# Kernel optimization log

Measured on AMD Instinct MI355X. Metric: run time of the kernel, lower is better.

The kernel has to match this reference:

```python
import jax, jax.numpy as jnp
import numpy as np

N_NODES = 140000   # 14 frames * 10000 nodes/frame
N_EDGES = 2240000  # avg degree 16
NFEAT = 128
NHID = 128
N_FRAMES = 14


def setup_inputs() -> dict:
    key = jax.random.key(0)
    k1, k2, k3, k4, k5 = jax.random.split(key, 5)
    x = jax.random.normal(k1, (N_NODES, NFEAT), dtype=jnp.float32)
    # gc1 parameters (only layer actually used in forward)
    W = jax.random.normal(k2, (NFEAT, NHID), dtype=jnp.float32) * 0.05
    b = jnp.zeros((NHID,), dtype=jnp.float32)
    # sparse normalized adjacency as COO edge list (row sorted for fast segment_sum)
    edge_row = jnp.sort(jax.random.randint(k3, (N_EDGES,), 0, N_NODES, dtype=jnp.int32))
    edge_col = jax.random.randint(k4, (N_EDGES,), 0, N_NODES, dtype=jnp.int32)
    edge_val = jax.random.uniform(k5, (N_EDGES,), dtype=jnp.float32)
    return {"x": x, "W": W, "b": b, "edge_val": edge_val,
            "edge_row": edge_row, "edge_col": edge_col}


def reference(x, W, b, edge_val, edge_row, edge_col):
    # GraphConvolution: adj @ (x @ W) + b  (adj sparse, COO)
    support = x @ W                                   # [N, NHID]
    msgs = edge_val[:, None] * support[edge_col]      # [E, NHID] gather
    agg = jax.ops.segment_sum(msgs, edge_row, num_segments=N_NODES,
                              indices_are_sorted=True)  # [N, NHID] scatter-add
    h = jax.nn.relu(agg + b)
    # view(14, -1, c) then max over frame axis
    h = h.reshape(N_FRAMES, -1, NHID)                 # [14, N/14, NHID]
    h = jnp.max(h, axis=0)                            # [N/14, NHID]
    return jax.nn.log_softmax(h, axis=1)
```

## Files before the change

kernel.cpp:

```cpp
#include <hip/hip_runtime.h>
#include <hip/hip_bf16.h>

#define N_NODES 140000
#define N_EDGES 2240000
#define NFEAT 128
#define NHID 128
#define N_FRAMES 14
#define NODES_PER_FRAME 10000
#define CAP 352

typedef __attribute__((ext_vector_type(8))) short frag_b16;
typedef __attribute__((ext_vector_type(4))) int frag_i4;
typedef __attribute__((ext_vector_type(4))) float f32x4;

__device__ __forceinline__ unsigned short f2bf(float f) {
    union { float f; unsigned int u; } v; v.f = f;
    unsigned int r = v.u + 0x7fffu + ((v.u >> 16) & 1u);
    return (unsigned short)(r >> 16);
}
__device__ __forceinline__ int pk_bf16(float a, float b) {
    union { __hip_bfloat162 h; int i; } u;
    u.h = __float22bfloat162_rn(make_float2(a, b));
    return u.i;
}
__device__ __forceinline__ float2 bf2x2(unsigned int u) {
    union { unsigned int u; float f; } lo, hi;
    lo.u = u << 16;
    hi.u = u & 0xffff0000u;
    return make_float2(lo.f, hi.f);
}

__global__ void prep_kernel(const float* __restrict__ W, unsigned short* __restrict__ WT,
                            const int* __restrict__ edge_row, int* __restrict__ row_ptr) {
    int e = blockIdx.x * blockDim.x + threadIdx.x;
    if (e < NFEAT * NHID) {
        int k = e >> 7, n = e & 127;
        WT[n * 128 + k] = f2bf(W[e]);
    }
    if (e < N_EDGES) {
        int r = edge_row[e];
        int prev = (e == 0) ? -1 : edge_row[e - 1];
        for (int q = prev + 1; q <= r; ++q) row_ptr[q] = e;
        if (e == N_EDGES - 1) {
            for (int q = r + 1; q <= N_NODES; ++q) row_ptr[q] = N_EDGES;
        }
    }
}

#define WT_STRIDE 136

__global__ __launch_bounds__(256) void gemm_kernel(
        const float* __restrict__ x, const unsigned short* __restrict__ WT,
        unsigned short* __restrict__ support) {
    __shared__ unsigned short wt_lds[128 * WT_STRIDE];

    const uint4* WTv = (const uint4*)WT;
    for (int idx = threadIdx.x; idx < 2048; idx += 256) {
        uint4 d = WTv[idx];
        int elem = idx << 3;
        int n = elem >> 7, k = elem & 127;
        *(uint4*)&wt_lds[n * WT_STRIDE + k] = d;
    }

    int wave = threadIdx.x >> 6;
    int lane = threadIdx.x & 63;
    int m = lane & 15;
    int q = lane >> 4;

    long row0 = (long)blockIdx.x * 64 + wave * 16;

    int arow = (int)row0 + m;
    if (arow >= N_NODES) arow = N_NODES - 1;
    const float* xrow = x + (long)arow * 128 + q * 8;
    frag_b16 xa[4];
#pragma unroll
    for (int ks = 0; ks < 4; ++ks) {
        float4 lo = *(const float4*)(xrow + ks * 32);
        float4 hi = *(const float4*)(xrow + ks * 32 + 4);
        union { frag_b16 f; frag_i4 i; } u;
        u.i[0] = pk_bf16(lo.x, lo.y);
        u.i[1] = pk_bf16(lo.z, lo.w);
        u.i[2] = pk_bf16(hi.x, hi.y);
        u.i[3] = pk_bf16(hi.z, hi.w);
        xa[ks] = u.f;
    }

    __syncthreads();

    if (row0 < N_NODES) {
        f32x4 acc[8];
#pragma unroll
        for (int t = 0; t < 8; ++t) acc[t] = (f32x4){0.f, 0.f, 0.f, 0.f};

#pragma unroll
        for (int t = 0; t < 8; ++t) {
            const unsigned short* bp = &wt_lds[(t * 16 + m) * WT_STRIDE + q * 8];
#pragma unroll
            for (int ks = 0; ks < 4; ++ks) {
                frag_b16 wfrag = *(const frag_b16*)(bp + ks * 32);
                acc[t] = __builtin_amdgcn_mfma_f32_16x16x32_bf16(wfrag, xa[ks], acc[t], 0, 0, 0);
            }
        }

        long node = row0 + m;
        if (node < N_NODES) {
            unsigned short* srow = support + node * 128;
#pragma unroll
            for (int t = 0; t < 8; ++t) {
                int2 pk;
                pk.x = pk_bf16(acc[t][0], acc[t][1]);
                pk.y = pk_bf16(acc[t][2], acc[t][3]);
                *(int2*)(srow + t * 16 + q * 4) = pk;
            }
        }
    }
}

__global__ __launch_bounds__(128) void agg_kernel(
        const unsigned short* __restrict__ support, const float* __restrict__ b,
        const float* __restrict__ edge_val, const int* __restrict__ edge_col,
        const int* __restrict__ row_ptr, float* __restrict__ out) {
    __shared__ int   segStart[2][8];
    __shared__ int   segLen[2][8];
    __shared__ int   segOff[2][8];
    __shared__ int2  eBuf[2][CAP];
    __shared__ float xch[2][64][2];

    const int i = blockIdx.x;
    const int lane = threadIdx.x & 63;
    const int w = threadIdx.x >> 6;
    const char* supB = (const char*)support;
    const unsigned lane4 = (unsigned)lane * 4u;

    int a = 0, len = 0;
    if (lane < 7) {
        int n = (w * 7 + lane) * NODES_PER_FRAME + i;
        a = row_ptr[n];
        len = row_ptr[n + 1] - a;
    }
    int len8 = (len + 7) & ~7;
    int off = 0;
#pragma unroll
    for (int f2 = 0; f2 < 7; ++f2) {
        int L2 = __shfl(len8, f2);
        if (f2 < lane) off += L2;
    }
    if (lane < 7) { segStart[w][lane] = a; segLen[w][lane] = len; segOff[w][lane] = off; }
    if (lane == 6) segOff[w][7] = off + len8;
    __syncthreads();

    const bool fit = segOff[w][7] <= CAP;

    if (fit) {
#pragma unroll 1
        for (int f = 0; f < 7; ++f) {
            int g = segStart[w][f], s = segOff[w][f], L = segLen[w][f];
            int L8 = (L + 7) & ~7;
            for (int j = lane; j < L8; j += 64) {
                int2 v;
                if (j < L) { v.x = edge_col[g + j]; v.y = __float_as_int(edge_val[g + j]); }
                else       { v.x = 0; v.y = 0; }
                eBuf[w][s + j] = v;
            }
        }
    }
    __syncthreads();

    const float2 bb = *(const float2*)&b[lane * 2];
    float2 mx = make_float2(0.f, 0.f);

    if (fit) {
#pragma unroll 1
        for (int f = 0; f < 7; ++f) {
            int s = segOff[w][f];
            int e8 = s + ((segLen[w][f] + 7) & ~7);
            float ax = 0.f, ay = 0.f;
            for (int j = s; j < e8; j += 8) {
                unsigned sv[8];
                float vv[8];
#pragma unroll
                for (int u = 0; u < 8; ++u) {
                    int2 ed = eBuf[w][j + u];
                    unsigned o = ((unsigned)ed.x << 8) + lane4;
                    sv[u] = *(const unsigned*)(supB + o);
                    vv[u] = __int_as_float(ed.y);
                }
#pragma unroll
                for (int u = 0; u < 8; ++u) {
                    float2 s2 = bf2x2(sv[u]);
                    ax = fmaf(vv[u], s2.x, ax);
                    ay = fmaf(vv[u], s2.y, ay);
                }
            }
            float hx = ax + bb.x, hy = ay + bb.y;
            mx.x = fmaxf(mx.x, hx > 0.f ? hx : 0.f);
            mx.y = fmaxf(mx.y, hy > 0.f ? hy : 0.f);
        }
    } else {
#pragma unroll 1
        for (int f = 0; f < 7; ++f) {
            int g = segStart[w][f], L = segLen[w][f];
            float ax = 0.f, ay = 0.f;
            for (int j = 0; j < L; ++j) {
                int c = edge_col[g + j];
                float v = edge_val[g + j];
                float2 s2 = bf2x2(*(const unsigned*)(supB + (((unsigned)c << 8) + lane4)));
                ax = fmaf(v, s2.x, ax);
                ay = fmaf(v, s2.y, ay);
            }
            float hx = ax + bb.x, hy = ay + bb.y;
            mx.x = fmaxf(mx.x, hx > 0.f ? hx : 0.f);
            mx.y = fmaxf(mx.y, hy > 0.f ? hy : 0.f);
        }
    }

    xch[w][lane][0] = mx.x;
    xch[w][lane][1] = mx.y;
    __syncthreads();
    float ox = fmaxf(xch[0][lane][0], xch[1][lane][0]);
    float oy = fmaxf(xch[0][lane][1], xch[1][lane][1]);

    float M = fmaxf(ox, oy);
#pragma unroll
    for (int o = 32; o >= 1; o >>= 1) M = fmaxf(M, __shfl_xor(M, o));
    float S = __expf(ox - M) + __expf(oy - M);
#pragma unroll
    for (int o = 32; o >= 1; o >>= 1) S += __shfl_xor(S, o);

    if (w == 0) {
        float ls = __logf(S);
        float2 o2 = make_float2((ox - M) - ls, (oy - M) - ls);
        *(float2*)&out[i * 128 + lane * 2] = o2;
    }
}

extern "C" void kernel_launch(void* const* d_in, const int* in_sizes, int n_in,
                              void* d_out, int out_size, void* d_ws, size_t ws_size,
                              hipStream_t stream) {
    const float* x        = (const float*)d_in[0];
    const float* W        = (const float*)d_in[1];
    const float* b        = (const float*)d_in[2];
    const float* edge_val = (const float*)d_in[3];
    const int*   edge_row = (const int*)d_in[4];
    const int*   edge_col = (const int*)d_in[5];
    float* out = (float*)d_out;

    char* ws = (char*)d_ws;
    unsigned short* support = (unsigned short*)ws;
    unsigned short* WT      = (unsigned short*)(ws + 35840000);
    int*            row_ptr = (int*)(ws + 35840000 + 32768);

    prep_kernel<<<(N_EDGES + 255) / 256, 256, 0, stream>>>(W, WT, edge_row, row_ptr);
    gemm_kernel<<<(N_NODES + 63) / 64, 256, 0, stream>>>(x, WT, support);
    agg_kernel<<<NODES_PER_FRAME, 128, 0, stream>>>(support, b, edge_val, edge_col, row_ptr, out);
}
```

Measured before the change: 221.4 us.

## Interleave seven frame segments per wave with software-pipelined gathers in aggregation

The aggregation kernel now stages each frame's edges into a fixed-size per-frame LDS slot array of 48 entries, replacing the variable-offset packed buffer and its prefix-sum and barrier. Each wave then walks all seven frame segments in lockstep, two edges per segment per step, and prefetches the next step's support rows before doing the current FMAs. This gives 14 independent gathers in flight per iteration and hides memory latency better than the serial per-frame loop. In exchange, short segments do padded zero work up to the longest segment, register pressure rises, and any wave with a segment longer than 48 takes the slow fallback path.

Result: slower. 226.6 us (+2.4%).

```diff
diff --git a/kernel.cpp b/kernel.cpp
--- a/kernel.cpp
+++ b/kernel.cpp
@@ -7,7 +7,7 @@
 #define NHID 128
 #define N_FRAMES 14
 #define NODES_PER_FRAME 10000
-#define CAP 352
+#define FSLOTS 48
 
 typedef __attribute__((ext_vector_type(8))) short frag_b16;
 typedef __attribute__((ext_vector_type(4))) int frag_i4;
@@ -120,17 +120,13 @@
         const unsigned short* __restrict__ support, const float* __restrict__ b,
         const float* __restrict__ edge_val, const int* __restrict__ edge_col,
         const int* __restrict__ row_ptr, float* __restrict__ out) {
-    __shared__ int   segStart[2][8];
-    __shared__ int   segLen[2][8];
-    __shared__ int   segOff[2][8];
-    __shared__ int2  eBuf[2][CAP];
+    __shared__ int2  eBuf[2][7][FSLOTS];
     __shared__ float xch[2][64][2];
 
     const int i = blockIdx.x;
     const int lane = threadIdx.x & 63;
     const int w = threadIdx.x >> 6;
-    const char* supB = (const char*)support;
-    const unsigned lane4 = (unsigned)lane * 4u;
+    const unsigned int* sup32 = (const unsigned int*)support;
 
     int a = 0, len = 0;
     if (lane < 7) {
@@ -138,80 +134,99 @@
         a = row_ptr[n];
         len = row_ptr[n + 1] - a;
     }
-    int len8 = (len + 7) & ~7;
-    int off = 0;
-#pragma unroll
-    for (int f2 = 0; f2 < 7; ++f2) {
-        int L2 = __shfl(len8, f2);
-        if (f2 < lane) off += L2;
-    }
-    if (lane < 7) { segStart[w][lane] = a; segLen[w][lane] = len; segOff[w][lane] = off; }
-    if (lane == 6) segOff[w][7] = off + len8;
-    __syncthreads();
-
-    const bool fit = segOff[w][7] <= CAP;
+    int ml = len;
+    ml = max(ml, __shfl_xor(ml, 1));
+    ml = max(ml, __shfl_xor(ml, 2));
+    ml = max(ml, __shfl_xor(ml, 4));
+    const int maxlen = __shfl(ml, 0);
+    const bool fit = maxlen <= FSLOTS;
 
     if (fit) {
+#pragma unroll
+        for (int f = 0; f < 7; ++f) {
+            int aF = __shfl(a, f), lF = __shfl(len, f);
+            if (lane < FSLOTS) {
+                int2 v = make_int2(0, 0);
+                if (lane < lF) {
+                    v.x = edge_col[aF + lane];
+                    v.y = __float_as_int(edge_val[aF + lane]);
+                }
+                eBuf[w][f][lane] = v;
+            }
+        }
+    }
+
+    const float2 bb = *(const float2*)&b[lane * 2];
+    float accx[7], accy[7];
+#pragma unroll
+    for (int f = 0; f < 7; ++f) { accx[f] = 0.f; accy[f] = 0.f; }
+
+    if (fit) {
+        const int R = (maxlen + 1) >> 1;
+        int4 cur[7];
+        unsigned sv0[7], sv1[7];
+
+#pragma unroll
+        for (int f = 0; f < 7; ++f) cur[f] = *(const int4*)&eBuf[w][f][0];
+#pragma unroll
+        for (int f = 0; f < 7; ++f) {
+            sv0[f] = sup32[((unsigned)cur[f].x << 6) | lane];
+            sv1[f] = sup32[((unsigned)cur[f].z << 6) | lane];
+        }
+
 #pragma unroll 1
-        for (int f = 0; f < 7; ++f) {
-            int g = segStart[w][f], s = segOff[w][f], L = segLen[w][f];
-            int L8 = (L + 7) & ~7;
-            for (int j = lane; j < L8; j += 64) {
-                int2 v;
-                if (j < L) { v.x = edge_col[g + j]; v.y = __float_as_int(edge_val[g + j]); }
-                else       { v.x = 0; v.y = 0; }
-                eBuf[w][s + j] = v;
-            }
-        }
-    }
-    __syncthreads();
-
-    const float2 bb = *(const float2*)&b[lane * 2];
-    float2 mx = make_float2(0.f, 0.f);
-
-    if (fit) {
-#pragma unroll 1
-        for (int f = 0; f < 7; ++f) {
-            int s = segOff[w][f];
-            int e8 = s + ((segLen[w][f] + 7) & ~7);
-            float ax = 0.f, ay = 0.f;
-            for (int j = s; j < e8; j += 8) {
-                unsigned sv[8];
-                float vv[8];
-#pragma unroll
-                for (int u = 0; u < 8; ++u) {
-                    int2 ed = eBuf[w][j + u];
-                    unsigned o = ((unsigned)ed.x << 8) + lane4;
-                    sv[u] = *(const unsigned*)(supB + o);
-                    vv[u] = __int_as_float(ed.y);
-                }
-#pragma unroll
-                for (int u = 0; u < 8; ++u) {
-                    float2 s2 = bf2x2(sv[u]);
-                    ax = fmaf(vv[u], s2.x, ax);
-                    ay = fmaf(vv[u], s2.y, ay);
-                }
-            }
-            float hx = ax + bb.x, hy = ay + bb.y;
-            mx.x = fmaxf(mx.x, hx > 0.f ? hx : 0.f);
-            mx.y = fmaxf(mx.y, hy > 0.f ? hy : 0.f);
+        for (int r = 0; r < R; ++r) {
+            int ro = (r + 1) * 2;
+            if (ro > FSLOTS - 2) ro = FSLOTS - 2;
+            int4 nxt[7];
+            unsigned nv0[7], nv1[7];
+#pragma unroll
+            for (int f = 0; f < 7; ++f) nxt[f] = *(const int4*)&eBuf[w][f][ro];
+#pragma unroll
+            for (int f = 0; f < 7; ++f) {
+                nv0[f] = sup32[((unsigned)nxt[f].x << 6) | lane];
+                nv1[f] = sup32[((unsigned)nxt[f].z << 6) | lane];
+            }
+#pragma unroll
+            for (int f = 0; f < 7; ++f) {
+                float v0 = __int_as_float(cur[f].y);
+                float v1 = __int_as_float(cur[f].w);
+                float2 s0 = bf2x2(sv0[f]);
+                float2 s1 = bf2x2(sv1[f]);
+                accx[f] = fmaf(v0, s0.x, accx[f]);
+                accy[f] = fmaf(v0, s0.y, accy[f]);
+                accx[f] = fmaf(v1, s1.x, accx[f]);
+                accy[f] = fmaf(v1, s1.y, accy[f]);
+            }
+#pragma unroll
+            for (int f = 0; f < 7; ++f) {
+                cur[f] = nxt[f];
+                sv0[f] = nv0[f];
+                sv1[f] = nv1[f];
+            }
         }
     } else {
 #pragma unroll 1
         for (int f = 0; f < 7; ++f) {
-            int g = segStart[w][f], L = segLen[w][f];
+            int aF = __shfl(a, f), lF = __shfl(len, f);
             float ax = 0.f, ay = 0.f;
-            for (int j = 0; j < L; ++j) {
-                int c = edge_col[g + j];
-                float v = edge_val[g + j];
-                float2 s2 = bf2x2(*(const unsigned*)(supB + (((unsigned)c << 8) + lane4)));
+            for (int j = 0; j < lF; ++j) {
+                int c = edge_col[aF + j];
+                float v = edge_val[aF + j];
+                float2 s2 = bf2x2(sup32[((unsigned)c << 6) | lane]);
                 ax = fmaf(v, s2.x, ax);
                 ay = fmaf(v, s2.y, ay);
             }
-            float hx = ax + bb.x, hy = ay + bb.y;
-            mx.x = fmaxf(mx.x, hx > 0.f ? hx : 0.f);
-            mx.y = fmaxf(mx.y, hy > 0.f ? hy : 0.f);
-        }
+            accx[f] = ax; accy[f] = ay;
+        }
+    }
+
+    float2 mx = make_float2(0.f, 0.f);
+#pragma unroll
+    for (int f = 0; f < 7; ++f) {
+        float hx = accx[f] + bb.x, hy = accy[f] + bb.y;
+        mx.x = fmaxf(mx.x, hx > 0.f ? hx : 0.f);
+        mx.y = fmaxf(mx.y, hy > 0.f ? hy : 0.f);
     }
 
     xch[w][lane][0] = mx.x;
```

## Quantize support to per-row int8 and split aggregation lanes across edges

Applied to the files above, without the earlier changes.

The GEMM epilogue now stores the support matrix as 8-bit values with a per-row absmax scale, offset by 128, instead of bf16. This halves the bytes gathered per edge in the aggregation. The aggregation folds each row's scale into the edge weight, and each half-wave handles alternate edges with 4 features per lane. The +128 offset is removed through a running sum of weights before the half-waves combine with a shuffle. Accuracy drops to about 8 bits per row, which may break tolerance, and each edge now needs an extra scale gather.

Result: faster. 198.7 us (-10.3%).

```diff
diff --git a/kernel.cpp b/kernel.cpp
--- a/kernel.cpp
+++ b/kernel.cpp
@@ -23,12 +23,6 @@
     u.h = __float22bfloat162_rn(make_float2(a, b));
     return u.i;
 }
-__device__ __forceinline__ float2 bf2x2(unsigned int u) {
-    union { unsigned int u; float f; } lo, hi;
-    lo.u = u << 16;
-    hi.u = u & 0xffff0000u;
-    return make_float2(lo.f, hi.f);
-}
 
 __global__ void prep_kernel(const float* __restrict__ W, unsigned short* __restrict__ WT,
                             const int* __restrict__ edge_row, int* __restrict__ row_ptr) {
@@ -51,7 +45,7 @@
 
 __global__ __launch_bounds__(256) void gemm_kernel(
         const float* __restrict__ x, const unsigned short* __restrict__ WT,
-        unsigned short* __restrict__ support) {
+        unsigned char* __restrict__ supQ, float* __restrict__ scales) {
     __shared__ unsigned short wt_lds[128 * WT_STRIDE];
 
     const uint4* WTv = (const uint4*)WT;
@@ -102,35 +96,48 @@
             }
         }
 
+        float amax = 0.f;
+#pragma unroll
+        for (int t = 0; t < 8; ++t)
+#pragma unroll
+            for (int r = 0; r < 4; ++r) amax = fmaxf(amax, fabsf(acc[t][r]));
+        amax = fmaxf(amax, __shfl_xor(amax, 16));
+        amax = fmaxf(amax, __shfl_xor(amax, 32));
+        float rinv = amax > 0.f ? 127.f / amax : 0.f;
+
         long node = row0 + m;
         if (node < N_NODES) {
-            unsigned short* srow = support + node * 128;
+            if (q == 0) scales[node] = amax * (1.f / 127.f);
+            unsigned char* srow = supQ + node * 128;
 #pragma unroll
             for (int t = 0; t < 8; ++t) {
-                int2 pk;
-                pk.x = pk_bf16(acc[t][0], acc[t][1]);
-                pk.y = pk_bf16(acc[t][2], acc[t][3]);
-                *(int2*)(srow + t * 16 + q * 4) = pk;
+                unsigned u0 = (unsigned)(rintf(acc[t][0] * rinv) + 128.f);
+                unsigned u1 = (unsigned)(rintf(acc[t][1] * rinv) + 128.f);
+                unsigned u2 = (unsigned)(rintf(acc[t][2] * rinv) + 128.f);
+                unsigned u3 = (unsigned)(rintf(acc[t][3] * rinv) + 128.f);
+                *(unsigned*)(srow + t * 16 + q * 4) = u0 | (u1 << 8) | (u2 << 16) | (u3 << 24);
             }
         }
     }
 }
 
 __global__ __launch_bounds__(128) void agg_kernel(
-        const unsigned short* __restrict__ support, const float* __restrict__ b,
+        const unsigned char* __restrict__ supQ, const float* __restrict__ scales,
+        const float* __restrict__ b,
         const float* __restrict__ edge_val, const int* __restrict__ edge_col,
         const int* __restrict__ row_ptr, float* __restrict__ out) {
-    __shared__ int   segStart[2][8];
-    __shared__ int   segLen[2][8];
-    __shared__ int   segOff[2][8];
-    __shared__ int2  eBuf[2][CAP];
-    __shared__ float xch[2][64][2];
+    __shared__ int    segStart[2][8];
+    __shared__ int    segLen[2][8];
+    __shared__ int    segOff[2][8];
+    __shared__ int2   eBuf[2][CAP];
+    __shared__ float4 xch[2][32];
 
     const int i = blockIdx.x;
     const int lane = threadIdx.x & 63;
     const int w = threadIdx.x >> 6;
-    const char* supB = (const char*)support;
-    const unsigned lane4 = (unsigned)lane * 4u;
+    const int eh = lane >> 5;
+    const int f4 = lane & 31;
+    const unsigned f4x4 = (unsigned)f4 * 4u;
 
     int a = 0, len = 0;
     if (lane < 7) {
@@ -157,80 +164,105 @@
             int g = segStart[w][f], s = segOff[w][f], L = segLen[w][f];
             int L8 = (L + 7) & ~7;
             for (int j = lane; j < L8; j += 64) {
-                int2 v;
-                if (j < L) { v.x = edge_col[g + j]; v.y = __float_as_int(edge_val[g + j]); }
-                else       { v.x = 0; v.y = 0; }
+                int2 v = make_int2(0, 0);
+                if (j < L) {
+                    int c = edge_col[g + j];
+                    v.x = c;
+                    v.y = __float_as_int(edge_val[g + j] * scales[c]);
+                }
                 eBuf[w][s + j] = v;
             }
         }
     }
     __syncthreads();
 
-    const float2 bb = *(const float2*)&b[lane * 2];
-    float2 mx = make_float2(0.f, 0.f);
+    const float4 bb = *(const float4*)&b[f4 * 4];
+    float4 mx = make_float4(0.f, 0.f, 0.f, 0.f);
 
     if (fit) {
 #pragma unroll 1
         for (int f = 0; f < 7; ++f) {
             int s = segOff[w][f];
             int e8 = s + ((segLen[w][f] + 7) & ~7);
-            float ax = 0.f, ay = 0.f;
+            float a0 = 0.f, a1 = 0.f, a2 = 0.f, a3 = 0.f, svf = 0.f;
             for (int j = s; j < e8; j += 8) {
-                unsigned sv[8];
-                float vv[8];
-#pragma unroll
-                for (int u = 0; u < 8; ++u) {
-                    int2 ed = eBuf[w][j + u];
-                    unsigned o = ((unsigned)ed.x << 8) + lane4;
-                    sv[u] = *(const unsigned*)(supB + o);
-                    vv[u] = __int_as_float(ed.y);
+                int2 ed[4];
+#pragma unroll
+                for (int p = 0; p < 4; ++p) ed[p] = eBuf[w][j + 2 * p + eh];
+                unsigned q4[4];
+#pragma unroll
+                for (int p = 0; p < 4; ++p)
+                    q4[p] = *(const unsigned*)(supQ + (((unsigned)ed[p].x) << 7) + f4x4);
+#pragma unroll
+                for (int p = 0; p < 4; ++p) {
+                    float vp = __int_as_float(ed[p].y);
+                    a0 = fmaf(vp, (float)( q4[p]        & 0xffu), a0);
+                    a1 = fmaf(vp, (float)((q4[p] >> 8)  & 0xffu), a1);
+                    a2 = fmaf(vp, (float)((q4[p] >> 16) & 0xffu), a2);
+                    a3 = fmaf(vp, (float)( q4[p] >> 24        ), a3);
+                    svf += vp;
                 }
-#pragma unroll
-                for (int u = 0; u < 8; ++u) {
-                    float2 s2 = bf2x2(sv[u]);
-                    ax = fmaf(vv[u], s2.x, ax);
-                    ay = fmaf(vv[u], s2.y, ay);
-                }
-            }
-            float hx = ax + bb.x, hy = ay + bb.y;
-            mx.x = fmaxf(mx.x, hx > 0.f ? hx : 0.f);
-            mx.y = fmaxf(mx.y, hy > 0.f ? hy : 0.f);
+            }
+            a0 += __shfl_xor(a0, 32); a1 += __shfl_xor(a1, 32);
+            a2 += __shfl_xor(a2, 32); a3 += __shfl_xor(a3, 32);
+            svf += __shfl_xor(svf, 32);
+            float h0 = fmaf(-128.f, svf, a0) + bb.x;
+            float h1 = fmaf(-128.f, svf, a1) + bb.y;
+            float h2 = fmaf(-128.f, svf, a2) + bb.z;
+            float h3 = fmaf(-128.f, svf, a3) + bb.w;
+            mx.x = fmaxf(mx.x, fmaxf(h0, 0.f));
+            mx.y = fmaxf(mx.y, fmaxf(h1, 0.f));
+            mx.z = fmaxf(mx.z, fmaxf(h2, 0.f));
+            mx.w = fmaxf(mx.w, fmaxf(h3, 0.f));
         }
     } else {
 #pragma unroll 1
         for (int f = 0; f < 7; ++f) {
             int g = segStart[w][f], L = segLen[w][f];
-            float ax = 0.f, ay = 0.f;
-            for (int j = 0; j < L; ++j) {
+            float a0 = 0.f, a1 = 0.f, a2 = 0.f, a3 = 0.f, svf = 0.f;
+            for (int j = eh; j < L; j += 2) {
                 int c = edge_col[g + j];
-                float v = edge_val[g + j];
-                float2 s2 = bf2x2(*(const unsigned*)(supB + (((unsigned)c << 8) + lane4)));
-                ax = fmaf(v, s2.x, ax);
-                ay = fmaf(v, s2.y, ay);
-            }
-            float hx = ax + bb.x, hy = ay + bb.y;
-            mx.x = fmaxf(mx.x, hx > 0.f ? hx : 0.f);
-            mx.y = fmaxf(mx.y, hy > 0.f ? hy : 0.f);
-        }
-    }
-
-    xch[w][lane][0] = mx.x;
-    xch[w][lane][1] = mx.y;
-    __syncthreads();
-    float ox = fmaxf(xch[0][lane][0], xch[1][lane][0]);
-    float oy = fmaxf(xch[0][lane][1], xch[1][lane][1]);
-
-    float M = fmaxf(ox, oy);
-#pragma unroll
-    for (int o = 32; o >= 1; o >>= 1) M = fmaxf(M, __shfl_xor(M, o));
-    float S = __expf(ox - M) + __expf(oy - M);
-#pragma unroll
-    for (int o = 32; o >= 1; o >>= 1) S += __shfl_xor(S, o);
-
-    if (w == 0) {
+                float vp = edge_val[g + j] * scales[c];
+                unsigned qv = *(const unsigned*)(supQ + (((unsigned)c) << 7) + f4x4);
+                a0 = fmaf(vp, (float)( qv        & 0xffu), a0);
+                a1 = fmaf(vp, (float)((qv >> 8)  & 0xffu), a1);
+                a2 = fmaf(vp, (float)((qv >> 16) & 0xffu), a2);
+                a3 = fmaf(vp, (float)( qv >> 24        ), a3);
+                svf += vp;
+            }
+            a0 += __shfl_xor(a0, 32); a1 += __shfl_xor(a1, 32);
+            a2 += __shfl_xor(a2, 32); a3 += __shfl_xor(a3, 32);
+            svf += __shfl_xor(svf, 32);
+            float h0 = fmaf(-128.f, svf, a0) + bb.x;
+            float h1 = fmaf(-128.f, svf, a1) + bb.y;
+            float h2 = fmaf(-128.f, svf, a2) + bb.z;
+            float h3 = fmaf(-128.f, svf, a3) + bb.w;
+            mx.x = fmaxf(mx.x, fmaxf(h0, 0.f));
+            mx.y = fmaxf(mx.y, fmaxf(h1, 0.f));
+            mx.z = fmaxf(mx.z, fmaxf(h2, 0.f));
+            mx.w = fmaxf(mx.w, fmaxf(h3, 0.f));
+        }
+    }
+
+    if (eh == 0) xch[w][f4] = mx;
+    __syncthreads();
+    float4 m0 = xch[0][f4], m1 = xch[1][f4];
+    float o0 = fmaxf(m0.x, m1.x);
+    float o1 = fmaxf(m0.y, m1.y);
+    float o2 = fmaxf(m0.z, m1.z);
+    float o3 = fmaxf(m0.w, m1.w);
+
+    float M = fmaxf(fmaxf(o0, o1), fmaxf(o2, o3));
+#pragma unroll
+    for (int o = 16; o >= 1; o >>= 1) M = fmaxf(M, __shfl_xor(M, o));
+    float S = __expf(o0 - M) + __expf(o1 - M) + __expf(o2 - M) + __expf(o3 - M);
+#pragma unroll
+    for (int o = 16; o >= 1; o >>= 1) S += __shfl_xor(S, o);
+
+    if (w == 0 && eh == 0) {
         float ls = __logf(S);
-        float2 o2 = make_float2((ox - M) - ls, (oy - M) - ls);
-        *(float2*)&out[i * 128 + lane * 2] = o2;
+        *(float4*)&out[i * 128 + f4 * 4] =
+            make_float4(o0 - M - ls, o1 - M - ls, o2 - M - ls, o3 - M - ls);
     }
 }
 
@@ -246,11 +278,12 @@
     float* out = (float*)d_out;
 
     char* ws = (char*)d_ws;
-    unsigned short* support = (unsigned short*)ws;
-    unsigned short* WT      = (unsigned short*)(ws + 35840000);
-    int*            row_ptr = (int*)(ws + 35840000 + 32768);
+    unsigned char*  supQ    = (unsigned char*)ws;
+    float*          scales  = (float*)(ws + 17920000);
+    unsigned short* WT      = (unsigned short*)(ws + 18480000);
+    int*            row_ptr = (int*)(ws + 18512768);
 
     prep_kernel<<<(N_EDGES + 255) / 256, 256, 0, stream>>>(W, WT, edge_row, row_ptr);
-    gemm_kernel<<<(N_NODES + 63) / 64, 256, 0, stream>>>(x, WT, support);
-    agg_kernel<<<NODES_PER_FRAME, 128, 0, stream>>>(support, b, edge_val, edge_col, row_ptr, out);
-}
+    gemm_kernel<<<(N_NODES + 63) / 64, 256, 0, stream>>>(x, WT, supQ, scales);
+    agg_kernel<<<NODES_PER_FRAME, 128, 0, stream>>>(supQ, scales, b, edge_val, edge_col, row_ptr, out);
+}
```
